# Performance work log

Measured on AMD Instinct MI355X. Metric: run time of the kernel, lower is better.

## Reference

```python
import jax, jax.numpy as jnp
import numpy as np

DIM = 768
HEADS = 12
DH = DIM // HEADS
SCALE = DH ** -0.5


def setup_inputs() -> dict:
    key = jax.random.key(0)
    ks = jax.random.split(key, 8)
    B, N = 8, 1024
    x = jax.random.normal(ks[0], (B, N, DIM), dtype=jnp.float32)
    rpb = jax.random.normal(ks[1], (1, HEADS, N, N), dtype=jnp.float32)
    s = DIM ** -0.5
    W_qkv = jax.random.normal(ks[2], (DIM, 3 * DIM), dtype=jnp.float32) * s
    W_out = jax.random.normal(ks[3], (DIM, DIM), dtype=jnp.float32) * s
    b_out = jnp.zeros((DIM,), dtype=jnp.float32)
    ln_g = jnp.ones((DIM,), dtype=jnp.float32)
    ln_b = jnp.zeros((DIM,), dtype=jnp.float32)
    return {"x": x, "relative_position_bias": rpb, "W_qkv": W_qkv,
            "W_out": W_out, "b_out": b_out, "ln_g": ln_g, "ln_b": ln_b}


def reference(x, relative_position_bias, W_qkv, W_out, b_out, ln_g, ln_b):
    # LayerNorm (eps matches torch default 1e-5)
    mu = jnp.mean(x, axis=-1, keepdims=True)
    var = jnp.mean(jnp.square(x - mu), axis=-1, keepdims=True)
    xn = (x - mu) * jax.lax.rsqrt(var + 1e-5) * ln_g + ln_b

    qkv = xn @ W_qkv                                  # [b,n,3*dim]
    q, k, v = jnp.split(qkv, 3, axis=-1)
    B, N, _ = x.shape
    reshape = lambda t: t.reshape(B, N, HEADS, DH).transpose(0, 2, 1, 3)  # b h n d
    q, k, v = reshape(q), reshape(k), reshape(v)

    scores = jnp.einsum('bhid,bhjd->bhij', q, k) * SCALE + relative_position_bias
    attn = jax.nn.softmax(scores, axis=-1)            # dropout p=0.0 -> identity
    out = jnp.einsum('bhij,bhjd->bhid', attn, v)
    out = out.transpose(0, 2, 1, 3).reshape(B, N, HEADS * DH)
    return out @ W_out + b_out
```

## Files before the change

### kernel.cpp

```cpp
#include <hip/hip_runtime.h>
#include <hip/hip_bf16.h>
#include <math.h>

#define BATCH 8
#define NSEQ  1024
#define DIMM  768
#define NHEAD 12
#define DHEAD 64
#define SCALE 0.125f
#define ROWS  (BATCH * NSEQ)

typedef __hip_bfloat16 bf16;
typedef __bf16 bf16x8 __attribute__((ext_vector_type(8)));
typedef float  f32x4  __attribute__((ext_vector_type(4)));

#if __has_builtin(__builtin_amdgcn_global_load_lds)
#define HAVE_GLL 1
typedef __attribute__((address_space(3))) void lds_void_t;
typedef const __attribute__((address_space(1))) void gbl_void_t;
__device__ __forceinline__ void gload16(const void* g, void* l) {
    __builtin_amdgcn_global_load_lds((gbl_void_t*)g, (lds_void_t*)l, 16, 0, 0);
}
#else
#define HAVE_GLL 0
#endif

__global__ __launch_bounds__(256) void ln_kernel(const float* __restrict__ x,
                                                 const float* __restrict__ g,
                                                 const float* __restrict__ bta,
                                                 bf16* __restrict__ y) {
    __shared__ float ps[4], pq[4];
    __shared__ float mean_s, rstd_s;
    int row = blockIdx.x;
    int tid = threadIdx.x;
    const float* xr = x + (size_t)row * DIMM;
    float v[3];
    float s = 0.f, sq = 0.f;
#pragma unroll
    for (int i = 0; i < 3; ++i) {
        v[i] = xr[tid + 256 * i];
        s += v[i];
        sq += v[i] * v[i];
    }
#pragma unroll
    for (int off = 32; off >= 1; off >>= 1) {
        s  += __shfl_down(s, off);
        sq += __shfl_down(sq, off);
    }
    int wid = tid >> 6, lane = tid & 63;
    if (lane == 0) { ps[wid] = s; pq[wid] = sq; }
    __syncthreads();
    if (tid == 0) {
        float S = ps[0] + ps[1] + ps[2] + ps[3];
        float Q = pq[0] + pq[1] + pq[2] + pq[3];
        float mean = S * (1.0f / DIMM);
        float var  = Q * (1.0f / DIMM) - mean * mean;
        mean_s = mean;
        rstd_s = rsqrtf(fmaxf(var, 0.f) + 1e-5f);
    }
    __syncthreads();
    float mean = mean_s, rstd = rstd_s;
    bf16* yr = y + (size_t)row * DIMM;
#pragma unroll
    for (int i = 0; i < 3; ++i) {
        int c = tid + 256 * i;
        yr[c] = __float2bfloat16((v[i] - mean) * rstd * g[c] + bta[c]);
    }
}

__global__ __launch_bounds__(256) void transpose_bf16(const float* __restrict__ W,
                                                      bf16* __restrict__ Wt,
                                                      int K, int N) {
    __shared__ float t[32][33];
    int n0 = blockIdx.x * 32, k0 = blockIdx.y * 32;
    int tx = threadIdx.x, ty = threadIdx.y;
#pragma unroll
    for (int i = 0; i < 32; i += 8)
        t[ty + i][tx] = W[(size_t)(k0 + ty + i) * N + n0 + tx];
    __syncthreads();
#pragma unroll
    for (int i = 0; i < 32; i += 8)
        Wt[(size_t)(n0 + ty + i) * K + k0 + tx] = __float2bfloat16(t[tx][ty + i]);
}

template <bool OUT_BF16>
__global__ __launch_bounds__(256) void gemm_mfma(const bf16* __restrict__ A,
                                                 const bf16* __restrict__ Bt,
                                                 const float* __restrict__ bias,
                                                 void* __restrict__ Cv,
                                                 int M, int Nn, int K) {
    __shared__ bf16 As[128][32];
    __shared__ bf16 Bs[128][32];
    int tid = threadIdx.x;
    int wave = tid >> 6, lane = tid & 63, quad = lane >> 4, l16 = lane & 15;
    int wm = (wave >> 1) * 64, wn = (wave & 1) * 64;
    int m0 = blockIdx.y * 128, n0 = blockIdx.x * 128;

    f32x4 acc[4][4] = {};

#if HAVE_GLL
    const char* Ag = (const char*)(A  + (size_t)(m0 + (tid >> 2)) * K + (tid & 3) * 8);
    const char* Bg = (const char*)(Bt + (size_t)(n0 + (tid >> 2)) * K + (tid & 3) * 8);
    char* AsB = (char*)&As[0][0] + tid * 16;
    char* BsB = (char*)&Bs[0][0] + tid * 16;
    const size_t radv = (size_t)64 * K * 2;

    for (int k0 = 0; k0 < K; k0 += 32) {
        __syncthreads();
        gload16(Ag, AsB);
        gload16(Ag + radv, AsB + 4096);
        gload16(Bg, BsB);
        gload16(Bg + radv, BsB + 4096);
        Ag += 64; Bg += 64;
        __syncthreads();
#else
    int srow = tid >> 1;
    int sk = (tid & 1) * 16;
    const bf16* Ap = A  + (size_t)(m0 + srow) * K + sk;
    const bf16* Bp = Bt + (size_t)(n0 + srow) * K + sk;
    for (int k0 = 0; k0 < K; k0 += 32) {
        uint4 a0 = *(const uint4*)(Ap + k0);
        uint4 a1 = *(const uint4*)(Ap + k0 + 8);
        uint4 b0 = *(const uint4*)(Bp + k0);
        uint4 b1 = *(const uint4*)(Bp + k0 + 8);
        __syncthreads();
        *(uint4*)&As[srow][sk]     = a0;
        *(uint4*)&As[srow][sk + 8] = a1;
        *(uint4*)&Bs[srow][sk]     = b0;
        *(uint4*)&Bs[srow][sk + 8] = b1;
        __syncthreads();
#endif
        bf16x8 af[4], bf_[4];
#pragma unroll
        for (int i = 0; i < 4; ++i) {
            af[i]  = *(const bf16x8*)&As[wm + i * 16 + l16][quad * 8];
            bf_[i] = *(const bf16x8*)&Bs[wn + i * 16 + l16][quad * 8];
        }
#pragma unroll
        for (int mi = 0; mi < 4; ++mi)
#pragma unroll
            for (int ni = 0; ni < 4; ++ni)
                acc[mi][ni] = __builtin_amdgcn_mfma_f32_16x16x32_bf16(
                    af[mi], bf_[ni], acc[mi][ni], 0, 0, 0);
    }

    float bv[4] = {0.f, 0.f, 0.f, 0.f};
    if (!OUT_BF16 && bias) {
#pragma unroll
        for (int ni = 0; ni < 4; ++ni) bv[ni] = bias[n0 + wn + ni * 16 + l16];
    }
#pragma unroll
    for (int mi = 0; mi < 4; ++mi)
#pragma unroll
        for (int reg = 0; reg < 4; ++reg) {
            size_t row = m0 + wm + mi * 16 + quad * 4 + reg;
#pragma unroll
            for (int ni = 0; ni < 4; ++ni) {
                int col = n0 + wn + ni * 16 + l16;
                float val = acc[mi][ni][reg] + bv[ni];
                if (OUT_BF16)
                    ((bf16*)Cv)[row * Nn + col] = __float2bfloat16(val);
                else
                    ((float*)Cv)[row * Nn + col] = val;
            }
        }
}

__global__ __launch_bounds__(256) void attn_mfma(const bf16* __restrict__ qkv,
                                                 const float* __restrict__ rpb,
                                                 bf16* __restrict__ outb) {
    __shared__ bf16 Ks[64][72];
    __shared__ unsigned Vt32[64][36];
    __shared__ bf16 Ps[4][16][72];

    int tid = threadIdx.x;
    int wave = tid >> 6, lane = tid & 63, quad = lane >> 4, l16 = lane & 15;
    int bid = blockIdx.x;
    int b  = bid & 7;
    int r2 = bid >> 3;
    int h  = r2 % NHEAD;
    int mt = r2 / NHEAD;
    int m0 = mt * 64;

    bf16x8 qf0, qf1;
    {
        const bf16* qrow = qkv + (size_t)(b * NSEQ + m0 + wave * 16 + l16) * (3 * DIMM) + h * DHEAD;
        qf0 = *(const bf16x8*)(qrow + quad * 8);
        qf1 = *(const bf16x8*)(qrow + 32 + quad * 8);
    }
    const float* rp = rpb + ((size_t)h * NSEQ + (m0 + wave * 16)) * NSEQ;

    bf16x8 onesf;
#pragma unroll
    for (int e = 0; e < 8; ++e) onesf[e] = (l16 == 0) ? (__bf16)1.0f : (__bf16)0.0f;

    float m_r[4];
    f32x4 accl = {0.f, 0.f, 0.f, 0.f};
    f32x4 acco[4] = {};
#pragma unroll
    for (int r = 0; r < 4; ++r) m_r[r] = -INFINITY;

    int srow = tid >> 2;
    int sd = (tid & 3) * 16;
    bool hi = (srow & 1);
    int p2 = srow >> 1;

    const bf16* kbase = qkv + (size_t)(b * NSEQ + srow) * (3 * DIMM) + DIMM + h * DHEAD + sd;
    uint4 kv0 = *(const uint4*)(kbase);
    uint4 kv1 = *(const uint4*)(kbase + 8);
    uint4 vv0 = *(const uint4*)(kbase + DIMM);
    uint4 vv1 = *(const uint4*)(kbase + DIMM + 8);

    for (int kt = 0; kt < 16; ++kt) {
        __syncthreads();
        *(uint4*)&Ks[srow][sd]     = kv0;
        *(uint4*)&Ks[srow][sd + 8] = kv1;
        {
            union { uint4 u4[2]; unsigned short us[16]; } vu;
            vu.u4[0] = vv0; vu.u4[1] = vv1;
            union { uint4 q; unsigned short h8[8]; } R, Sd;
            Sd.q = hi ? vu.u4[0] : vu.u4[1];
            R.q.x = __shfl_xor(Sd.q.x, 4);
            R.q.y = __shfl_xor(Sd.q.y, 4);
            R.q.z = __shfl_xor(Sd.q.z, 4);
            R.q.w = __shfl_xor(Sd.q.w, 4);
            if (!hi) {
#pragma unroll
                for (int j = 0; j < 8; ++j)
                    Vt32[sd + j][p2] = (unsigned)vu.us[j] | ((unsigned)R.h8[j] << 16);
            } else {
#pragma unroll
                for (int j = 0; j < 8; ++j)
                    Vt32[sd + 8 + j][p2] = (unsigned)R.h8[j] | ((unsigned)vu.us[8 + j] << 16);
            }
        }
        __syncthreads();

        if (kt + 1 < 16) {
            const bf16* kb2 = kbase + (size_t)(kt + 1) * 64 * (3 * DIMM);
            kv0 = *(const uint4*)(kb2);
            kv1 = *(const uint4*)(kb2 + 8);
            vv0 = *(const uint4*)(kb2 + DIMM);
            vv1 = *(const uint4*)(kb2 + DIMM + 8);
        }
        float rv[4][4];
        const float* rpk = rp + kt * 64;
#pragma unroll
        for (int t = 0; t < 4; ++t)
#pragma unroll
            for (int r = 0; r < 4; ++r)
                rv[t][r] = rpk[(size_t)(quad * 4 + r) * NSEQ + t * 16 + l16];

        f32x4 accs[4] = {};
#pragma unroll
        for (int t = 0; t < 4; ++t) {
            bf16x8 kf0 = *(const bf16x8*)&Ks[t * 16 + l16][quad * 8];
            bf16x8 kf1 = *(const bf16x8*)&Ks[t * 16 + l16][32 + quad * 8];
            accs[t] = __builtin_amdgcn_mfma_f32_16x16x32_bf16(qf0, kf0, accs[t], 0, 0, 0);
            accs[t] = __builtin_amdgcn_mfma_f32_16x16x32_bf16(qf1, kf1, accs[t], 0, 0, 0);
        }

        float sv[4][4], mx[4];
#pragma unroll
        for (int r = 0; r < 4; ++r) mx[r] = -INFINITY;
#pragma unroll
        for (int t = 0; t < 4; ++t)
#pragma unroll
            for (int r = 0; r < 4; ++r) {
                float s = accs[t][r] * SCALE + rv[t][r];
                sv[t][r] = s;
                mx[r] = fmaxf(mx[r], s);
            }
#pragma unroll
        for (int off = 1; off < 16; off <<= 1)
#pragma unroll
            for (int r = 0; r < 4; ++r) mx[r] = fmaxf(mx[r], __shfl_xor(mx[r], off));
        float alpha[4];
#pragma unroll
        for (int r = 0; r < 4; ++r) {
            float nm = fmaxf(m_r[r], mx[r]);
            alpha[r] = __expf(m_r[r] - nm);
            m_r[r] = nm;
        }
#pragma unroll
        for (int t = 0; t < 4; ++t)
#pragma unroll
            for (int r = 0; r < 4; ++r)
                sv[t][r] = __expf(sv[t][r] - m_r[r]);
#pragma unroll
        for (int r = 0; r < 4; ++r) accl[r] *= alpha[r];
#pragma unroll
        for (int dt = 0; dt < 4; ++dt)
#pragma unroll
            for (int r = 0; r < 4; ++r) acco[dt][r] *= alpha[r];

#pragma unroll
        for (int t = 0; t < 4; ++t)
#pragma unroll
            for (int r = 0; r < 4; ++r)
                Ps[wave][quad * 4 + r][t * 16 + l16] = __float2bfloat16(sv[t][r]);
        __asm__ volatile("s_waitcnt lgkmcnt(0)" ::: "memory");

        const bf16* VtB = (const bf16*)&Vt32[0][0];
#pragma unroll
        for (int s = 0; s < 2; ++s) {
            bf16x8 pf = *(const bf16x8*)&Ps[wave][l16][s * 32 + quad * 8];
            accl = __builtin_amdgcn_mfma_f32_16x16x32_bf16(pf, onesf, accl, 0, 0, 0);
#pragma unroll
            for (int dt = 0; dt < 4; ++dt) {
                bf16x8 vf = *(const bf16x8*)(VtB + (size_t)(dt * 16 + l16) * 72 + s * 32 + quad * 8);
                acco[dt] = __builtin_amdgcn_mfma_f32_16x16x32_bf16(pf, vf, acco[dt], 0, 0, 0);
            }
        }
    }

    float invl[4];
#pragma unroll
    for (int r = 0; r < 4; ++r) {
        float ls = __shfl(accl[r], lane & 48);
        invl[r] = 1.f / ls;
    }
    bf16* orow = outb + (size_t)(b * NSEQ + m0 + wave * 16) * DIMM + h * DHEAD;
#pragma unroll
    for (int dt = 0; dt < 4; ++dt)
#pragma unroll
        for (int r = 0; r < 4; ++r)
            orow[(size_t)(quad * 4 + r) * DIMM + dt * 16 + l16] =
                __float2bfloat16(acco[dt][r] * invl[r]);
}

extern "C" void kernel_launch(void* const* d_in, const int* in_sizes, int n_in,
                              void* d_out, int out_size, void* d_ws, size_t ws_size,
                              hipStream_t stream) {
    const float* x     = (const float*)d_in[0];
    const float* rpb   = (const float*)d_in[1];
    const float* W_qkv = (const float*)d_in[2];
    const float* W_out = (const float*)d_in[3];
    const float* b_out = (const float*)d_in[4];
    const float* ln_g  = (const float*)d_in[5];
    const float* ln_b  = (const float*)d_in[6];
    float* out = (float*)d_out;

    char* p = (char*)d_ws;
    bf16* xn    = (bf16*)p; p += (size_t)ROWS * DIMM * 2;
    bf16* qkv   = (bf16*)p; p += (size_t)ROWS * 3 * DIMM * 2;
    bf16* attn  = (bf16*)p; p += (size_t)ROWS * DIMM * 2;
    bf16* WqkvT = (bf16*)p; p += (size_t)3 * DIMM * DIMM * 2;
    bf16* WoutT = (bf16*)p; p += (size_t)DIMM * DIMM * 2;

    ln_kernel<<<ROWS, 256, 0, stream>>>(x, ln_g, ln_b, xn);
    transpose_bf16<<<dim3(3 * DIMM / 32, DIMM / 32), dim3(32, 8), 0, stream>>>(
        W_qkv, WqkvT, DIMM, 3 * DIMM);
    transpose_bf16<<<dim3(DIMM / 32, DIMM / 32), dim3(32, 8), 0, stream>>>(
        W_out, WoutT, DIMM, DIMM);

    gemm_mfma<true><<<dim3(3 * DIMM / 128, ROWS / 128), 256, 0, stream>>>(
        xn, WqkvT, nullptr, qkv, ROWS, 3 * DIMM, DIMM);

    attn_mfma<<<BATCH * NHEAD * (NSEQ / 64), 256, 0, stream>>>(qkv, rpb, attn);

    gemm_mfma<false><<<dim3(DIMM / 128, ROWS / 128), 256, 0, stream>>>(
        attn, WoutT, b_out, out, ROWS, DIMM, DIMM);
}
```

Before: 290.8 us.

## Restructure attention kernel: transposed QK^T, direct K loads, swizzled V tile

The attention kernel now computes S^T by swapping the MFMA operands, so each lane holds one query row. Row max and sum then need only two cross-lane shuffles, and the bias is read as contiguous float4 loads. K fragments are loaded straight from global memory instead of being staged in LDS, the V transpose buffer uses an XOR swizzle to avoid bank conflicts, and the ones-matrix MFMA used for the row sum is replaced by scalar accumulation. It also sets a minimum of 5 blocks per SM in the launch bounds, which caps register use and risks spills; the uncached per-wave K loads may raise global traffic.

```diff
diff --git a/kernel.cpp b/kernel.cpp
--- a/kernel.cpp
+++ b/kernel.cpp
@@ -24,6 +24,13 @@
 #else
 #define HAVE_GLL 0
 #endif
+
+__device__ __forceinline__ unsigned pk2(float a, float b) {
+    union { unsigned u; bf16 h[2]; } x;
+    x.h[0] = __float2bfloat16(a);
+    x.h[1] = __float2bfloat16(b);
+    return x.u;
+}
 
 __global__ __launch_bounds__(256) void ln_kernel(const float* __restrict__ x,
                                                  const float* __restrict__ g,
@@ -166,10 +173,9 @@
         }
 }
 
-__global__ __launch_bounds__(256) void attn_mfma(const bf16* __restrict__ qkv,
-                                                 const float* __restrict__ rpb,
-                                                 bf16* __restrict__ outb) {
-    __shared__ bf16 Ks[64][72];
+__global__ __launch_bounds__(256, 5) void attn_mfma(const bf16* __restrict__ qkv,
+                                                    const float* __restrict__ rpb,
+                                                    bf16* __restrict__ outb) {
     __shared__ unsigned Vt32[64][36];
     __shared__ bf16 Ps[4][16][72];
 
@@ -182,133 +188,116 @@
     int mt = r2 / NHEAD;
     int m0 = mt * 64;
 
-    bf16x8 qf0, qf1;
-    {
-        const bf16* qrow = qkv + (size_t)(b * NSEQ + m0 + wave * 16 + l16) * (3 * DIMM) + h * DHEAD;
-        qf0 = *(const bf16x8*)(qrow + quad * 8);
-        qf1 = *(const bf16x8*)(qrow + 32 + quad * 8);
-    }
-    const float* rp = rpb + ((size_t)h * NSEQ + (m0 + wave * 16)) * NSEQ;
-
-    bf16x8 onesf;
-#pragma unroll
-    for (int e = 0; e < 8; ++e) onesf[e] = (l16 == 0) ? (__bf16)1.0f : (__bf16)0.0f;
-
-    float m_r[4];
-    f32x4 accl = {0.f, 0.f, 0.f, 0.f};
+    const bf16* qrow = qkv + (size_t)(b * NSEQ + m0 + wave * 16 + l16) * (3 * DIMM) + h * DHEAD;
+    bf16x8 qf0 = *(const bf16x8*)(qrow + quad * 8);
+    bf16x8 qf1 = *(const bf16x8*)(qrow + 32 + quad * 8);
+
+    const float* rp = rpb + ((size_t)h * NSEQ + (m0 + wave * 16 + l16)) * NSEQ;
+
+    const bf16* kg = qkv + (size_t)(b * NSEQ + l16) * (3 * DIMM) + DIMM + h * DHEAD + quad * 8;
+
+    int vk = (tid >> 3) * 2;
+    int vd = (tid & 7) * 8;
+    int vkp = tid >> 3;
+    const bf16* vg = qkv + (size_t)(b * NSEQ + vk) * (3 * DIMM) + 2 * DIMM + h * DHEAD + vd;
+    uint4 va = *(const uint4*)(vg);
+    uint4 vb = *(const uint4*)(vg + 3 * DIMM);
+
+    float m_s = -INFINITY, l_s = 0.f;
     f32x4 acco[4] = {};
-#pragma unroll
-    for (int r = 0; r < 4; ++r) m_r[r] = -INFINITY;
-
-    int srow = tid >> 2;
-    int sd = (tid & 3) * 16;
-    bool hi = (srow & 1);
-    int p2 = srow >> 1;
-
-    const bf16* kbase = qkv + (size_t)(b * NSEQ + srow) * (3 * DIMM) + DIMM + h * DHEAD + sd;
-    uint4 kv0 = *(const uint4*)(kbase);
-    uint4 kv1 = *(const uint4*)(kbase + 8);
-    uint4 vv0 = *(const uint4*)(kbase + DIMM);
-    uint4 vv1 = *(const uint4*)(kbase + DIMM + 8);
+
+    int wblk = ((vkp >> 2) ^ (vd >> 3)) << 2 | (vkp & 3);
 
     for (int kt = 0; kt < 16; ++kt) {
         __syncthreads();
-        *(uint4*)&Ks[srow][sd]     = kv0;
-        *(uint4*)&Ks[srow][sd + 8] = kv1;
         {
-            union { uint4 u4[2]; unsigned short us[16]; } vu;
-            vu.u4[0] = vv0; vu.u4[1] = vv1;
-            union { uint4 q; unsigned short h8[8]; } R, Sd;
-            Sd.q = hi ? vu.u4[0] : vu.u4[1];
-            R.q.x = __shfl_xor(Sd.q.x, 4);
-            R.q.y = __shfl_xor(Sd.q.y, 4);
-            R.q.z = __shfl_xor(Sd.q.z, 4);
-            R.q.w = __shfl_xor(Sd.q.w, 4);
-            if (!hi) {
-#pragma unroll
-                for (int j = 0; j < 8; ++j)
-                    Vt32[sd + j][p2] = (unsigned)vu.us[j] | ((unsigned)R.h8[j] << 16);
-            } else {
-#pragma unroll
-                for (int j = 0; j < 8; ++j)
-                    Vt32[sd + 8 + j][p2] = (unsigned)R.h8[j] | ((unsigned)vu.us[8 + j] << 16);
+            union { uint4 q; unsigned short u[8]; } A_, B_;
+            A_.q = va; B_.q = vb;
+#pragma unroll
+            for (int j = 0; j < 8; ++j)
+                Vt32[vd + j][wblk] = (unsigned)A_.u[j] | ((unsigned)B_.u[j] << 16);
+        }
+        __syncthreads();
+
+        if (kt + 1 < 16) {
+            const bf16* v2 = vg + (size_t)(kt + 1) * 64 * (3 * DIMM);
+            va = *(const uint4*)(v2);
+            vb = *(const uint4*)(v2 + 3 * DIMM);
+        }
+
+        float4 rv[4];
+        const float* rpk = rp + kt * 64;
+#pragma unroll
+        for (int t = 0; t < 4; ++t)
+            rv[t] = *(const float4*)&rpk[t * 16 + quad * 4];
+
+        f32x4 accs[4] = {};
+#pragma unroll
+        for (int t = 0; t < 4; ++t) {
+            const bf16* kr = kg + (size_t)(kt * 64 + t * 16) * (3 * DIMM);
+            bf16x8 kf0 = *(const bf16x8*)(kr);
+            bf16x8 kf1 = *(const bf16x8*)(kr + 32);
+            accs[t] = __builtin_amdgcn_mfma_f32_16x16x32_bf16(kf0, qf0, accs[t], 0, 0, 0);
+            accs[t] = __builtin_amdgcn_mfma_f32_16x16x32_bf16(kf1, qf1, accs[t], 0, 0, 0);
+        }
+
+        float mx = -INFINITY;
+        {
+            float rb[4][4] = {{rv[0].x, rv[0].y, rv[0].z, rv[0].w},
+                              {rv[1].x, rv[1].y, rv[1].z, rv[1].w},
+                              {rv[2].x, rv[2].y, rv[2].z, rv[2].w},
+                              {rv[3].x, rv[3].y, rv[3].z, rv[3].w}};
+#pragma unroll
+            for (int t = 0; t < 4; ++t)
+#pragma unroll
+                for (int r = 0; r < 4; ++r) {
+                    accs[t][r] = fmaf(accs[t][r], SCALE, rb[t][r]);
+                    mx = fmaxf(mx, accs[t][r]);
+                }
+        }
+        mx = fmaxf(mx, __shfl_xor(mx, 16));
+        mx = fmaxf(mx, __shfl_xor(mx, 32));
+        float mn = fmaxf(m_s, mx);
+        float alpha = __expf(m_s - mn);
+        m_s = mn;
+        float sum = 0.f;
+#pragma unroll
+        for (int t = 0; t < 4; ++t)
+#pragma unroll
+            for (int r = 0; r < 4; ++r) {
+                float p = __expf(accs[t][r] - mn);
+                accs[t][r] = p;
+                sum += p;
             }
-        }
-        __syncthreads();
-
-        if (kt + 1 < 16) {
-            const bf16* kb2 = kbase + (size_t)(kt + 1) * 64 * (3 * DIMM);
-            kv0 = *(const uint4*)(kb2);
-            kv1 = *(const uint4*)(kb2 + 8);
-            vv0 = *(const uint4*)(kb2 + DIMM);
-            vv1 = *(const uint4*)(kb2 + DIMM + 8);
-        }
-        float rv[4][4];
-        const float* rpk = rp + kt * 64;
-#pragma unroll
-        for (int t = 0; t < 4; ++t)
-#pragma unroll
-            for (int r = 0; r < 4; ++r)
-                rv[t][r] = rpk[(size_t)(quad * 4 + r) * NSEQ + t * 16 + l16];
-
-        f32x4 accs[4] = {};
+        sum += __shfl_xor(sum, 16);
+        sum += __shfl_xor(sum, 32);
+        l_s = l_s * alpha + sum;
+
+        float ab[4];
+#pragma unroll
+        for (int r = 0; r < 4; ++r) ab[r] = __shfl(alpha, quad * 4 + r);
+#pragma unroll
+        for (int dt = 0; dt < 4; ++dt)
+#pragma unroll
+            for (int r = 0; r < 4; ++r) acco[dt][r] *= ab[r];
+
 #pragma unroll
         for (int t = 0; t < 4; ++t) {
-            bf16x8 kf0 = *(const bf16x8*)&Ks[t * 16 + l16][quad * 8];
-            bf16x8 kf1 = *(const bf16x8*)&Ks[t * 16 + l16][32 + quad * 8];
-            accs[t] = __builtin_amdgcn_mfma_f32_16x16x32_bf16(qf0, kf0, accs[t], 0, 0, 0);
-            accs[t] = __builtin_amdgcn_mfma_f32_16x16x32_bf16(qf1, kf1, accs[t], 0, 0, 0);
-        }
-
-        float sv[4][4], mx[4];
-#pragma unroll
-        for (int r = 0; r < 4; ++r) mx[r] = -INFINITY;
-#pragma unroll
-        for (int t = 0; t < 4; ++t)
-#pragma unroll
-            for (int r = 0; r < 4; ++r) {
-                float s = accs[t][r] * SCALE + rv[t][r];
-                sv[t][r] = s;
-                mx[r] = fmaxf(mx[r], s);
-            }
-#pragma unroll
-        for (int off = 1; off < 16; off <<= 1)
-#pragma unroll
-            for (int r = 0; r < 4; ++r) mx[r] = fmaxf(mx[r], __shfl_xor(mx[r], off));
-        float alpha[4];
-#pragma unroll
-        for (int r = 0; r < 4; ++r) {
-            float nm = fmaxf(m_r[r], mx[r]);
-            alpha[r] = __expf(m_r[r] - nm);
-            m_r[r] = nm;
-        }
-#pragma unroll
-        for (int t = 0; t < 4; ++t)
-#pragma unroll
-            for (int r = 0; r < 4; ++r)
-                sv[t][r] = __expf(sv[t][r] - m_r[r]);
-#pragma unroll
-        for (int r = 0; r < 4; ++r) accl[r] *= alpha[r];
-#pragma unroll
-        for (int dt = 0; dt < 4; ++dt)
-#pragma unroll
-            for (int r = 0; r < 4; ++r) acco[dt][r] *= alpha[r];
-
-#pragma unroll
-        for (int t = 0; t < 4; ++t)
-#pragma unroll
-            for (int r = 0; r < 4; ++r)
-                Ps[wave][quad * 4 + r][t * 16 + l16] = __float2bfloat16(sv[t][r]);
+            uint2 w;
+            w.x = pk2(accs[t][0], accs[t][1]);
+            w.y = pk2(accs[t][2], accs[t][3]);
+            *(uint2*)&Ps[wave][l16][t * 16 + quad * 4] = w;
+        }
         __asm__ volatile("s_waitcnt lgkmcnt(0)" ::: "memory");
 
-        const bf16* VtB = (const bf16*)&Vt32[0][0];
 #pragma unroll
         for (int s = 0; s < 2; ++s) {
             bf16x8 pf = *(const bf16x8*)&Ps[wave][l16][s * 32 + quad * 8];
-            accl = __builtin_amdgcn_mfma_f32_16x16x32_bf16(pf, onesf, accl, 0, 0, 0);
 #pragma unroll
             for (int dt = 0; dt < 4; ++dt) {
-                bf16x8 vf = *(const bf16x8*)(VtB + (size_t)(dt * 16 + l16) * 72 + s * 32 + quad * 8);
+                int row = dt * 16 + l16;
+                int sblk = ((s * 4 + quad) ^ ((row >> 3) & 7)) << 2;
+                bf16x8 vf = *(const bf16x8*)&Vt32[row][sblk];
                 acco[dt] = __builtin_amdgcn_mfma_f32_16x16x32_bf16(pf, vf, acco[dt], 0, 0, 0);
             }
         }
@@ -316,10 +305,7 @@
 
     float invl[4];
 #pragma unroll
-    for (int r = 0; r < 4; ++r) {
-        float ls = __shfl(accl[r], lane & 48);
-        invl[r] = 1.f / ls;
-    }
+    for (int r = 0; r < 4; ++r) invl[r] = 1.f / __shfl(l_s, quad * 4 + r);
     bf16* orow = outb + (size_t)(b * NSEQ + m0 + wave * 16) * DIMM + h * DHEAD;
 #pragma unroll
     for (int dt = 0; dt < 4; ++dt)
```

Measured after the change: 358.2 us. 1.23x slower.
